# Kernel optimization log

Hardware: AMD Instinct MI355X
Metric: run time of the kernel (lower is better)

The kernel has to match this reference:

```python
import jax, jax.numpy as jnp
import numpy as np

B, C, H, W = 512, 256, 9, 9
HEADS, K = 4, 9
D_K = C // HEADS
EPS = 1e-5


def setup_inputs() -> dict:
    key = jax.random.key(0)
    ks = jax.random.split(key, 8)
    s = 1.0 / np.sqrt(C)
    return {
        "x": jax.random.normal(ks[0], (B, C, H, W), jnp.float32),
        "wq": jax.random.normal(ks[1], (C, C), jnp.float32) * s,
        "bq": jax.random.normal(ks[2], (C,), jnp.float32) * s,
        "wk": jax.random.normal(ks[3], (C, C), jnp.float32) * s,
        "bk": jax.random.normal(ks[4], (C,), jnp.float32) * s,
        "wv": jax.random.normal(ks[5], (C, C), jnp.float32) * s,
        "bv": jax.random.normal(ks[6], (C,), jnp.float32) * s,
        "a": jax.random.normal(ks[7], (HEADS, D_K), jnp.float32),
        "gamma": jnp.ones((C,), jnp.float32),
        "beta": jnp.zeros((C,), jnp.float32),
    }


def reference(x, wq, bq, wk, bk, wv, bv, a, gamma, beta):
    N = H * W  # 81 tokens
    tokens = x.reshape(B, C, N).transpose(0, 2, 1)  # [B, N, C]

    # pairwise euclidean distances (cdist)
    sq = jnp.sum(tokens * tokens, axis=-1)  # [B, N]
    d2 = sq[:, :, None] + sq[:, None, :] - 2.0 * jnp.einsum("bnc,bmc->bnm", tokens, tokens)
    dist = jnp.sqrt(jnp.maximum(d2, 0.0))  # [B, N, N]

    # k nearest neighbors (smallest distance)
    _, idx = jax.lax.top_k(-dist, K)  # idx: [B, N, K]

    # gather neighbor features: [B, N, K, C]
    nbr = jax.vmap(lambda t, i: t[i])(tokens, idx)

    q = tokens @ wq.T + bq                      # [B, N, C]
    kf = nbr @ wk.T + bk                        # [B, N, K, C]
    comb = jax.nn.leaky_relu(q[:, :, None, :] + kf, 0.2)
    comb = comb.reshape(B, N, K, HEADS, D_K)
    scores = jnp.einsum("bnkhd,hd->bnkh", comb, a)
    attn = jax.nn.softmax(scores, axis=2)       # over K neighbors
    v = (nbr @ wv.T + bv).reshape(B, N, K, HEADS, D_K)
    out = jnp.einsum("bnkh,bnkhd->bnhd", attn, v).reshape(B, N, C)
    out = out.transpose(0, 2, 1).reshape(B, C, H, W)

    # BatchNorm2d (training-mode batch statistics, biased variance)
    mean = jnp.mean(out, axis=(0, 2, 3))
    var = jnp.var(out, axis=(0, 2, 3))
    bn = (out - mean[None, :, None, None]) * jax.lax.rsqrt(var + EPS)[None, :, None, None]
    bn = bn * gamma[None, :, None, None] + beta[None, :, None, None]
    return jax.nn.relu(bn + x)
```

## Files before the change

kernel.cpp:

```cpp
#include <hip/hip_runtime.h>
#include <hip/hip_bf16.h>

#define B_   512
#define C_   256
#define N_   81
#define M_   (B_ * N_)
#define KNN  9

typedef __attribute__((ext_vector_type(8))) short short8;
typedef __attribute__((ext_vector_type(4))) float f32x4;
typedef __attribute__((ext_vector_type(4))) ushort u16x4;

#define GLD16(g, l) __builtin_amdgcn_global_load_lds(                      \
    (const __attribute__((address_space(1))) void*)(g),                    \
    (__attribute__((address_space(3))) void*)(l), 16, 0, 0)

__device__ __forceinline__ float bf2f(ushort u) {
  union { uint i; float f; } c; c.i = (uint)u << 16; return c.f;
}
__device__ __forceinline__ ushort f2bf(float f) {
  __hip_bfloat16 h = __float2bfloat16(f); return *(ushort*)&h;
}

__global__ __launch_bounds__(256) void split_kernel(
    const float* __restrict__ x, ushort* __restrict__ tokb,
    char* __restrict__ lobuf,
    const float* __restrict__ wq, const float* __restrict__ bq,
    const float* __restrict__ wk, const float* __restrict__ bk,
    const float* __restrict__ wv, const float* __restrict__ bv,
    ushort* __restrict__ wcat, float* __restrict__ bcat) {
  __shared__ __align__(16) float raw[32 * 81];
  const int bid = blockIdx.x;
  const int tid = threadIdx.x;
  if (bid >= 4096) {
    const int j = bid - 4096, c = tid;
    const int sel = j >> 8, jr = j & 255;
    const float* W  = sel == 0 ? wq : (sel == 1 ? wk : wv);
    const float* Bb = sel == 0 ? bq : (sel == 1 ? bk : bv);
    wcat[(size_t)j * 256 + c] = f2bf(W[jr * 256 + c]);
    if (c == 0) bcat[j] = Bb[jr];
    return;
  }
  const int b = bid >> 3, ch = bid & 7;
  const float* src = x + (size_t)b * (C_ * N_) + ch * 32 * N_;
#pragma unroll
  for (int it = 0; it < 3; ++it) {
    int e4 = tid + it * 256;
    if (e4 < 648) *(f32x4*)&raw[e4 * 4] = *(const f32x4*)&src[e4 * 4];
  }
  char* dst = lobuf + (size_t)bid * 6144;
  __syncthreads();
#pragma unroll
  for (int it = 0; it < 6; ++it) {
    int p = tid + it * 256;
    if (p < 1296) {
      int n = p >> 4, q = p & 15;
      float v0 = raw[(2 * q) * N_ + n];
      float v1 = raw[(2 * q + 1) * N_ + n];
      __hip_bfloat16 h0 = __float2bfloat16(v0);
      __hip_bfloat16 h1 = __float2bfloat16(v1);
      float r0 = v0 - __bfloat162float(h0);
      float r1 = v1 - __bfloat162float(h1);
      __hip_bfloat16 g0 = __float2bfloat16(r0);
      __hip_bfloat16 g1 = __float2bfloat16(r1);
      uint hp = (uint)(*(ushort*)&h0) | ((uint)(*(ushort*)&h1) << 16);
      uint lp = (uint)(*(ushort*)&g0) | ((uint)(*(ushort*)&g1) << 16);
      int off = (((q >> 2) << 4) ^ (((n >> 1) & 3) << 4)) + ((q & 3) << 2);
      *(uint*)(dst + n * 64 + off) = lp;
      *(uint*)&tokb[((size_t)(b * N_ + n)) * 256 + ch * 32 + 2 * q] = hp;
    }
  }
}

__global__ __launch_bounds__(256) void knn_kernel(
    const ushort* __restrict__ tokb, const char* __restrict__ lobuf,
    int* __restrict__ knn_idx) {
  __shared__ __align__(16) char smem[31488];
  __shared__ float sqv[96];
  const int b = blockIdx.x;
  const int tid = threadIdx.x;
  const int w = tid >> 6, lane = tid & 63;
  const int wr = w >> 1, wc = w & 1;
  const int l15 = lane & 15;
  const int g16 = lane >> 4;

  const char* tb = (const char*)(tokb + (size_t)b * N_ * 256);
  const char* lb = lobuf + (size_t)b * 8 * 6144;

#pragma unroll
  for (int it = 0; it < 3; ++it) {
    int idx = it * 256 + tid;
    if (idx < 384) {
      int n = idx >> 2, gp = idx & 3;
      int g = gp ^ ((n >> 1) & 3);
      GLD16(tb + (size_t)n * 512 + (g << 4), smem + idx * 16);
    } else {
      GLD16(lb + (idx - 384) * 16, smem + idx * 16);
    }
  }

  f32x4 acc[3][3];
#pragma unroll
  for (int i = 0; i < 3; ++i)
#pragma unroll
    for (int j = 0; j < 3; ++j) acc[i][j] = {0.f, 0.f, 0.f, 0.f};

#pragma unroll
  for (int ch = 0; ch < 8; ++ch) {
    char* cur = smem + (ch & 1) * 12288;
    char* nxt = smem + ((ch + 1) & 1) * 12288;
    if (ch < 7) {
#pragma unroll
      for (int it = 0; it < 3; ++it) {
        int idx = it * 256 + tid;
        if (idx < 384) {
          int n = idx >> 2, gp = idx & 3;
          int g = gp ^ ((n >> 1) & 3);
          GLD16(tb + (size_t)n * 512 + (ch + 1) * 64 + (g << 4),
                nxt + idx * 16);
        } else {
          GLD16(lb + (size_t)(ch + 1) * 6144 + (idx - 384) * 16,
                nxt + idx * 16);
        }
      }
      asm volatile("s_waitcnt vmcnt(3)" ::: "memory");
    } else {
      asm volatile("s_waitcnt vmcnt(0)" ::: "memory");
    }
    __builtin_amdgcn_s_barrier();
    __builtin_amdgcn_sched_barrier(0);
    short8 ah[3], al[3], bh[3], bl[3];
#pragma unroll
    for (int i = 0; i < 3; ++i) {
      int ra = wr * 48 + i * 16 + l15;
      int oa = ra * 64 + ((g16 << 4) ^ (((ra >> 1) & 3) << 4));
      ah[i] = *(const short8*)(cur + oa);
      al[i] = *(const short8*)(cur + 6144 + oa);
      int rb = wc * 48 + i * 16 + l15;
      int ob = rb * 64 + ((g16 << 4) ^ (((rb >> 1) & 3) << 4));
      bh[i] = *(const short8*)(cur + ob);
      bl[i] = *(const short8*)(cur + 6144 + ob);
    }
#pragma unroll
    for (int i = 0; i < 3; ++i)
#pragma unroll
      for (int j = 0; j < 3; ++j) {
        acc[i][j] = __builtin_amdgcn_mfma_f32_16x16x32_bf16(
            ah[i], bh[j], acc[i][j], 0, 0, 0);
        acc[i][j] = __builtin_amdgcn_mfma_f32_16x16x32_bf16(
            ah[i], bl[j], acc[i][j], 0, 0, 0);
        acc[i][j] = __builtin_amdgcn_mfma_f32_16x16x32_bf16(
            al[i], bh[j], acc[i][j], 0, 0, 0);
        acc[i][j] = __builtin_amdgcn_mfma_f32_16x16x32_bf16(
            al[i], bl[j], acc[i][j], 0, 0, 0);
      }
    __builtin_amdgcn_sched_barrier(0);
    __builtin_amdgcn_s_barrier();
  }
  float* G = (float*)smem;
#pragma unroll
  for (int i = 0; i < 3; ++i) {
    const int row0 = wr * 48 + i * 16 + ((lane >> 4) << 2);
#pragma unroll
    for (int j = 0; j < 3; ++j) {
      const int col = wc * 48 + j * 16 + l15;
#pragma unroll
      for (int reg = 0; reg < 4; ++reg) {
        const int row = row0 + reg;
        if (row < N_) G[row * 97 + col] = acc[i][j][reg];
      }
    }
  }
  __syncthreads();
  if (tid < N_) sqv[tid] = G[tid * 97 + tid];
  __syncthreads();
  if (tid < N_) {
    const int n = tid;
    const float sn = sqv[n];
    const float* grow = &G[n * 97];
    float bd[KNN]; int bi[KNN];
#pragma unroll
    for (int k = 0; k < KNN; ++k) { bd[k] = 3.4e38f; bi[k] = 0; }
    for (int m = 0; m < N_; ++m) {
      float d2 = sn + sqv[m] - 2.f * grow[m];
      float wv = bd[0]; int wi = 0;
#pragma unroll
      for (int k = 1; k < KNN; ++k) {
        bool g_ = bd[k] > wv;
        wv = g_ ? bd[k] : wv;
        wi = g_ ? k : wi;
      }
      bool repl = d2 < wv;
#pragma unroll
      for (int k = 0; k < KNN; ++k) {
        bool here = repl & (wi == k);
        bd[k] = here ? d2 : bd[k];
        bi[k] = here ? m : bi[k];
      }
    }
#pragma unroll
    for (int k = 0; k < KNN; ++k)
      knn_idx[((size_t)b * N_ + n) * KNN + k] = bi[k];
  }
}

__global__ __launch_bounds__(256) void qkv_mfma_kernel(
    const ushort* __restrict__ tokb, const ushort* __restrict__ wcat,
    const float* __restrict__ bcat, ushort* __restrict__ qkvb) {
  __shared__ ushort At[128 * 64];
  __shared__ ushort Bt[128 * 64];
  const int bid = blockIdx.x;
  const int xcd = bid & 7, li = bid >> 3;
  const int mt = xcd * 41 + li / 6;
  if (mt >= 324) return;
  const int m0 = mt * 128;
  const int j0 = (li % 6) * 128;
  const int tid = threadIdx.x;
  const int w = tid >> 6, lane = tid & 63;
  const int wr = w >> 1, wc = w & 1;

  const char* pA[4]; const char* pB[4]; int oL[4];
#pragma unroll
  for (int it = 0; it < 4; ++it) {
    int o = (it * 256 + tid) * 16;
    int r = o >> 7, cp = o & 127;
    int cl = cp ^ ((r & 7) << 4);
    oL[it] = o;
    pA[it] = (const char*)tokb + ((size_t)(m0 + r) * 256) * 2 + cl;
    pB[it] = (const char*)wcat + ((size_t)(j0 + r) * 256) * 2 + cl;
  }

  f32x4 acc[4][4];
#pragma unroll
  for (int i = 0; i < 4; ++i)
#pragma unroll
    for (int j = 0; j < 4; ++j) acc[i][j] = {0.f, 0.f, 0.f, 0.f};

  const int l15 = lane & 15;
  const int sw = (lane & 7) << 4;
  const int kgrp = (lane >> 4) << 4;

  for (int k0 = 0; k0 < 256; k0 += 64) {
    __syncthreads();
#pragma unroll
    for (int it = 0; it < 4; ++it) {
      GLD16(pA[it] + k0 * 2, (char*)At + oL[it]);
      GLD16(pB[it] + k0 * 2, (char*)Bt + oL[it]);
    }
    __syncthreads();
#pragma unroll
    for (int kk = 0; kk < 2; ++kk) {
      const int cb = (kk * 64 + kgrp) ^ sw;
      short8 am[4], bn[4];
#pragma unroll
      for (int i = 0; i < 4; ++i) {
        const int ra = wr * 64 + i * 16 + l15;
        am[i] = *(const short8*)((const char*)At + ra * 128 + cb);
        const int rb = wc * 64 + i * 16 + l15;
        bn[i] = *(const short8*)((const char*)Bt + rb * 128 + cb);
      }
#pragma unroll
      for (int i = 0; i < 4; ++i)
#pragma unroll
        for (int j = 0; j < 4; ++j)
          acc[i][j] = __builtin_amdgcn_mfma_f32_16x16x32_bf16(
              am[i], bn[j], acc[i][j], 0, 0, 0);
    }
  }

#pragma unroll
  for (int j = 0; j < 4; ++j) {
    const int colj = j0 + wc * 64 + j * 16 + l15;
    const float bs = bcat[colj];
#pragma unroll
    for (int i = 0; i < 4; ++i) {
      const int rowm = m0 + wr * 64 + i * 16 + ((lane >> 4) << 2);
#pragma unroll
      for (int reg = 0; reg < 4; ++reg)
        qkvb[(size_t)(rowm + reg) * 768 + colj] = f2bf(acc[i][j][reg] + bs);
    }
  }
}

__global__ __launch_bounds__(256) void attn_kernel(
    const ushort* __restrict__ qkvc, const int* __restrict__ knn_idx,
    const float* __restrict__ a, ushort* __restrict__ qkvb) {
  const int nwg = M_ / 4;
  const int bid = blockIdx.x;
  const int swz = (bid & 7) * (nwg / 8) + (bid >> 3);
  const int w = threadIdx.x >> 6, lane = threadIdx.x & 63;
  const int m = swz * 4 + w;
  const int b = m / N_;
  const int bbase = b * N_;

  int nbk_l = 0;
  if (lane < KNN) nbk_l = knn_idx[(size_t)m * KNN + lane];

  const u16x4 qu = *(const u16x4*)&qkvc[(size_t)m * 768 + lane * 4];
  const f32x4 a4 = *(const f32x4*)&a[lane * 4];
  float q4[4];
#pragma unroll
  for (int u = 0; u < 4; ++u) q4[u] = bf2f(qu[u]);

  float sc[KNN];
  int nb[KNN];
#pragma unroll
  for (int k = 0; k < KNN; ++k) {
    const int nbk = __builtin_amdgcn_readlane(nbk_l, k);
    nb[k] = nbk;
    const ushort* krow = qkvc + (size_t)(bbase + nbk) * 768 + 256;
    const u16x4 ku = *(const u16x4*)&krow[lane * 4];
    float p = 0.f;
#pragma unroll
    for (int u = 0; u < 4; ++u) {
      float t = q4[u] + bf2f(ku[u]);
      t = fmaxf(t, 0.2f * t);
      p = __builtin_fmaf(t, a4[u], p);
    }
    p += __shfl_xor(p, 1, 16);
    p += __shfl_xor(p, 2, 16);
    p += __shfl_xor(p, 4, 16);
    p += __shfl_xor(p, 8, 16);
    sc[k] = p;
  }
  float mx = sc[0];
#pragma unroll
  for (int k = 1; k < KNN; ++k) mx = fmaxf(mx, sc[k]);
  float s = 0.f;
#pragma unroll
  for (int k = 0; k < KNN; ++k) {
    sc[k] = __builtin_amdgcn_exp2f((sc[k] - mx) * 1.44269504f);
    s += sc[k];
  }
  const float inv = __builtin_amdgcn_rcpf(s);
  f32x4 acc = {0.f, 0.f, 0.f, 0.f};
#pragma unroll
  for (int k = 0; k < KNN; ++k) {
    const ushort* vrow = qkvc + (size_t)(bbase + nb[k]) * 768 + 512;
    const u16x4 vu = *(const u16x4*)&vrow[lane * 4];
    const float wk_ = sc[k] * inv;
#pragma unroll
    for (int u = 0; u < 4; ++u)
      acc[u] = __builtin_fmaf(wk_, bf2f(vu[u]), acc[u]);
  }
  u16x4 o;
#pragma unroll
  for (int u = 0; u < 4; ++u) o[u] = f2bf(acc[u]);
  *(u16x4*)&qkvb[(size_t)m * 768 + lane * 4] = o;
}

__global__ __launch_bounds__(256) void bn_partial_kernel(
    const ushort* __restrict__ qkvb, float* __restrict__ ps,
    float* __restrict__ ps2) {
  const int g = blockIdx.x, c = threadIdx.x;
  float s = 0.f, s2 = 0.f;
  for (int r = 0; r < M_ / 256; ++r) {
    float v = bf2f(qkvb[((size_t)g * (M_ / 256) + r) * 768 + c]);
    s += v; s2 += v * v;
  }
  ps[g * 256 + c] = s;
  ps2[g * 256 + c] = s2;
}

__global__ __launch_bounds__(256) void bn_finalize_kernel(
    const float* __restrict__ ps, const float* __restrict__ ps2,
    const float* __restrict__ gamma, const float* __restrict__ beta,
    float* __restrict__ scale, float* __restrict__ shift) {
  const int c = threadIdx.x;
  float s = 0.f, s2 = 0.f;
  for (int g = 0; g < 256; ++g) { s += ps[g * 256 + c]; s2 += ps2[g * 256 + c]; }
  const float mean = s * (1.f / (float)M_);
  const float var = s2 * (1.f / (float)M_) - mean * mean;
  const float rstd = rsqrtf(var + 1e-5f);
  scale[c] = gamma[c] * rstd;
  shift[c] = beta[c] - mean * gamma[c] * rstd;
}

__global__ __launch_bounds__(256) void bn_apply_kernel(
    const ushort* __restrict__ qkvb, const float* __restrict__ x,
    const float* __restrict__ scale, const float* __restrict__ shift,
    float* __restrict__ y) {
  __shared__ float t[N_ * 65];
  const int b = blockIdx.x, tid = threadIdx.x;
  for (int c0 = 0; c0 < 256; c0 += 64) {
    __syncthreads();
    for (int e = tid; e < N_ * 64; e += 256) {
      int n = e >> 6, c = e & 63;
      t[n * 65 + c] = bf2f(qkvb[((size_t)b * N_ + n) * 768 + c0 + c]);
    }
    __syncthreads();
    for (int f = tid; f < 64 * N_; f += 256) {
      int c = f / N_, n = f - c * N_;
      float o = t[n * 65 + c];
      size_t gi = (size_t)b * (C_ * N_) + (size_t)(c0 + c) * N_ + n;
      float bn = o * scale[c0 + c] + shift[c0 + c];
      float v = bn + x[gi];
      y[gi] = v > 0.f ? v : 0.f;
    }
  }
}

extern "C" void kernel_launch(void* const* d_in, const int* in_sizes, int n_in,
                              void* d_out, int out_size, void* d_ws,
                              size_t ws_size, hipStream_t stream) {
  const float* x     = (const float*)d_in[0];
  const float* wq    = (const float*)d_in[1];
  const float* bq    = (const float*)d_in[2];
  const float* wk    = (const float*)d_in[3];
  const float* bk    = (const float*)d_in[4];
  const float* wv    = (const float*)d_in[5];
  const float* bv    = (const float*)d_in[6];
  const float* a     = (const float*)d_in[7];
  const float* gamma = (const float*)d_in[8];
  const float* beta  = (const float*)d_in[9];
  float* out = (float*)d_out;

  ushort* qkvb = (ushort*)d_ws;
  char*   lobuf = (char*)qkvb;
  ushort* tokb = qkvb + (size_t)M_ * 768;
  ushort* wcat = tokb + (size_t)M_ * 256;
  float*  bcat = (float*)(wcat + 768 * 256);
  int*    kidx = (int*)(bcat + 768);
  float*  ps   = (float*)(kidx + (size_t)M_ * KNN);
  float*  ps2  = ps + 256 * 256;
  float*  scale = ps2 + 256 * 256;
  float*  shift = scale + 256;

  split_kernel<<<4096 + 768, 256, 0, stream>>>(
      x, tokb, lobuf, wq, bq, wk, bk, wv, bv, wcat, bcat);
  knn_kernel<<<B_, 256, 0, stream>>>(tokb, lobuf, kidx);
  qkv_mfma_kernel<<<1968, 256, 0, stream>>>(tokb, wcat, bcat, qkvb);
  attn_kernel<<<M_ / 4, 256, 0, stream>>>(qkvb, kidx, a, qkvb);
  bn_partial_kernel<<<256, 256, 0, stream>>>(qkvb, ps, ps2);
  bn_finalize_kernel<<<1, 256, 0, stream>>>(ps, ps2, gamma, beta, scale, shift);
  bn_apply_kernel<<<B_, 256, 0, stream>>>(qkvb, x, scale, shift, out);
}
```

Measured before the change: 160.8 us.

## Fuse attention with per-batch BN partial statistics and write compact output buffer

The attention kernel now runs one 1024-thread block per batch item, with 16 waves covering all 81 tokens. Outputs are staged in shared memory so the block can compute per-channel sum and sum-of-squares partials directly, which removes the separate bn_partial pass over global memory. Output is also written to a compact 256-stride buffer instead of the 768-stride qkv buffer, so bn_apply reads contiguous rows. In exchange, the finalize kernel must reduce 512 partials instead of 256, and the large blocks with 6-iteration per-wave loops may lower occupancy and latency hiding compared with the earlier fine-grained grid.

```diff
diff --git a/kernel.cpp b/kernel.cpp
--- a/kernel.cpp
+++ b/kernel.cpp
@@ -282,84 +282,96 @@
   }
 }
 
-__global__ __launch_bounds__(256) void attn_kernel(
+__global__ __launch_bounds__(1024) void attn_bn_kernel(
     const ushort* __restrict__ qkvc, const int* __restrict__ knn_idx,
-    const float* __restrict__ a, ushort* __restrict__ qkvb) {
-  const int nwg = M_ / 4;
+    const float* __restrict__ a, ushort* __restrict__ outNC,
+    float* __restrict__ ps, float* __restrict__ ps2) {
+  __shared__ __align__(16) char obuf[N_ * 512];
+  __shared__ float psl[2][256], psl2[2][256];
   const int bid = blockIdx.x;
-  const int swz = (bid & 7) * (nwg / 8) + (bid >> 3);
-  const int w = threadIdx.x >> 6, lane = threadIdx.x & 63;
-  const int m = swz * 4 + w;
-  const int b = m / N_;
+  const int b = (bid & 7) * 64 + (bid >> 3);
+  const int tid = threadIdx.x;
+  const int w = tid >> 6, lane = tid & 63;
   const int bbase = b * N_;
-
-  int nbk_l = 0;
-  if (lane < KNN) nbk_l = knn_idx[(size_t)m * KNN + lane];
-
-  const u16x4 qu = *(const u16x4*)&qkvc[(size_t)m * 768 + lane * 4];
   const f32x4 a4 = *(const f32x4*)&a[lane * 4];
-  float q4[4];
-#pragma unroll
-  for (int u = 0; u < 4; ++u) q4[u] = bf2f(qu[u]);
-
-  float sc[KNN];
-  int nb[KNN];
-#pragma unroll
-  for (int k = 0; k < KNN; ++k) {
-    const int nbk = __builtin_amdgcn_readlane(nbk_l, k);
-    nb[k] = nbk;
-    const ushort* krow = qkvc + (size_t)(bbase + nbk) * 768 + 256;
-    const u16x4 ku = *(const u16x4*)&krow[lane * 4];
-    float p = 0.f;
-#pragma unroll
-    for (int u = 0; u < 4; ++u) {
-      float t = q4[u] + bf2f(ku[u]);
-      t = fmaxf(t, 0.2f * t);
-      p = __builtin_fmaf(t, a4[u], p);
-    }
-    p += __shfl_xor(p, 1, 16);
-    p += __shfl_xor(p, 2, 16);
-    p += __shfl_xor(p, 4, 16);
-    p += __shfl_xor(p, 8, 16);
-    sc[k] = p;
-  }
-  float mx = sc[0];
-#pragma unroll
-  for (int k = 1; k < KNN; ++k) mx = fmaxf(mx, sc[k]);
-  float s = 0.f;
-#pragma unroll
-  for (int k = 0; k < KNN; ++k) {
-    sc[k] = __builtin_amdgcn_exp2f((sc[k] - mx) * 1.44269504f);
-    s += sc[k];
-  }
-  const float inv = __builtin_amdgcn_rcpf(s);
-  f32x4 acc = {0.f, 0.f, 0.f, 0.f};
-#pragma unroll
-  for (int k = 0; k < KNN; ++k) {
-    const ushort* vrow = qkvc + (size_t)(bbase + nb[k]) * 768 + 512;
-    const u16x4 vu = *(const u16x4*)&vrow[lane * 4];
-    const float wk_ = sc[k] * inv;
-#pragma unroll
-    for (int u = 0; u < 4; ++u)
-      acc[u] = __builtin_fmaf(wk_, bf2f(vu[u]), acc[u]);
-  }
-  u16x4 o;
-#pragma unroll
-  for (int u = 0; u < 4; ++u) o[u] = f2bf(acc[u]);
-  *(u16x4*)&qkvb[(size_t)m * 768 + lane * 4] = o;
-}
-
-__global__ __launch_bounds__(256) void bn_partial_kernel(
-    const ushort* __restrict__ qkvb, float* __restrict__ ps,
-    float* __restrict__ ps2) {
-  const int g = blockIdx.x, c = threadIdx.x;
-  float s = 0.f, s2 = 0.f;
-  for (int r = 0; r < M_ / 256; ++r) {
-    float v = bf2f(qkvb[((size_t)g * (M_ / 256) + r) * 768 + c]);
-    s += v; s2 += v * v;
-  }
-  ps[g * 256 + c] = s;
-  ps2[g * 256 + c] = s2;
+
+  for (int r = 0; r < 6; ++r) {
+    const int tok = w + 16 * r;
+    if (tok < N_) {
+      const int m = bbase + tok;
+      int nbk_l = 0;
+      if (lane < KNN) nbk_l = knn_idx[(size_t)m * KNN + lane];
+
+      const u16x4 qu = *(const u16x4*)&qkvc[(size_t)m * 768 + lane * 4];
+      float q4[4];
+#pragma unroll
+      for (int u = 0; u < 4; ++u) q4[u] = bf2f(qu[u]);
+
+      float sc[KNN];
+      int nb[KNN];
+#pragma unroll
+      for (int k = 0; k < KNN; ++k) {
+        const int nbk = __builtin_amdgcn_readlane(nbk_l, k);
+        nb[k] = nbk;
+        const ushort* krow = qkvc + (size_t)(bbase + nbk) * 768 + 256;
+        const u16x4 ku = *(const u16x4*)&krow[lane * 4];
+        float p = 0.f;
+#pragma unroll
+        for (int u = 0; u < 4; ++u) {
+          float t = q4[u] + bf2f(ku[u]);
+          t = fmaxf(t, 0.2f * t);
+          p = __builtin_fmaf(t, a4[u], p);
+        }
+        p += __shfl_xor(p, 1, 16);
+        p += __shfl_xor(p, 2, 16);
+        p += __shfl_xor(p, 4, 16);
+        p += __shfl_xor(p, 8, 16);
+        sc[k] = p;
+      }
+      float mx = sc[0];
+#pragma unroll
+      for (int k = 1; k < KNN; ++k) mx = fmaxf(mx, sc[k]);
+      float s = 0.f;
+#pragma unroll
+      for (int k = 0; k < KNN; ++k) {
+        sc[k] = __builtin_amdgcn_exp2f((sc[k] - mx) * 1.44269504f);
+        s += sc[k];
+      }
+      const float inv = __builtin_amdgcn_rcpf(s);
+      f32x4 acc = {0.f, 0.f, 0.f, 0.f};
+#pragma unroll
+      for (int k = 0; k < KNN; ++k) {
+        const ushort* vrow = qkvc + (size_t)(bbase + nb[k]) * 768 + 512;
+        const u16x4 vu = *(const u16x4*)&vrow[lane * 4];
+        const float wk_ = sc[k] * inv;
+#pragma unroll
+        for (int u = 0; u < 4; ++u)
+          acc[u] = __builtin_fmaf(wk_, bf2f(vu[u]), acc[u]);
+      }
+      u16x4 o;
+#pragma unroll
+      for (int u = 0; u < 4; ++u) o[u] = f2bf(acc[u]);
+      *(u16x4*)(obuf + tok * 512 + lane * 8) = o;
+      *(u16x4*)&outNC[(size_t)m * 256 + lane * 4] = o;
+    }
+  }
+  __syncthreads();
+  if (tid < 512) {
+    const int half = tid >> 8, c = tid & 255;
+    const int rbeg = half * 41, rend = half ? 81 : 41;
+    float s = 0.f, s2 = 0.f;
+    for (int rr = rbeg; rr < rend; ++rr) {
+      float v = bf2f(*(const ushort*)(obuf + rr * 512 + c * 2));
+      s += v; s2 = __builtin_fmaf(v, v, s2);
+    }
+    psl[half][c] = s;
+    psl2[half][c] = s2;
+  }
+  __syncthreads();
+  if (tid < 256) {
+    ps[b * 256 + tid] = psl[0][tid] + psl[1][tid];
+    ps2[b * 256 + tid] = psl2[0][tid] + psl2[1][tid];
+  }
 }
 
 __global__ __launch_bounds__(256) void bn_finalize_kernel(
@@ -368,7 +380,7 @@
     float* __restrict__ scale, float* __restrict__ shift) {
   const int c = threadIdx.x;
   float s = 0.f, s2 = 0.f;
-  for (int g = 0; g < 256; ++g) { s += ps[g * 256 + c]; s2 += ps2[g * 256 + c]; }
+  for (int g = 0; g < 512; ++g) { s += ps[g * 256 + c]; s2 += ps2[g * 256 + c]; }
   const float mean = s * (1.f / (float)M_);
   const float var = s2 * (1.f / (float)M_) - mean * mean;
   const float rstd = rsqrtf(var + 1e-5f);
@@ -377,7 +389,7 @@
 }
 
 __global__ __launch_bounds__(256) void bn_apply_kernel(
-    const ushort* __restrict__ qkvb, const float* __restrict__ x,
+    const ushort* __restrict__ outNC, const float* __restrict__ x,
     const float* __restrict__ scale, const float* __restrict__ shift,
     float* __restrict__ y) {
   __shared__ float t[N_ * 65];
@@ -386,7 +398,7 @@
     __syncthreads();
     for (int e = tid; e < N_ * 64; e += 256) {
       int n = e >> 6, c = e & 63;
-      t[n * 65 + c] = bf2f(qkvb[((size_t)b * N_ + n) * 768 + c0 + c]);
+      t[n * 65 + c] = bf2f(outNC[((size_t)b * N_ + n) * 256 + c0 + c]);
     }
     __syncthreads();
     for (int f = tid; f < 64 * N_; f += 256) {
@@ -422,16 +434,16 @@
   float*  bcat = (float*)(wcat + 768 * 256);
   int*    kidx = (int*)(bcat + 768);
   float*  ps   = (float*)(kidx + (size_t)M_ * KNN);
-  float*  ps2  = ps + 256 * 256;
-  float*  scale = ps2 + 256 * 256;
+  float*  ps2  = ps + 512 * 256;
+  float*  scale = ps2 + 512 * 256;
   float*  shift = scale + 256;
+  ushort* outNC = (ushort*)(shift + 256);
 
   split_kernel<<<4096 + 768, 256, 0, stream>>>(
       x, tokb, lobuf, wq, bq, wk, bk, wv, bv, wcat, bcat);
   knn_kernel<<<B_, 256, 0, stream>>>(tokb, lobuf, kidx);
   qkv_mfma_kernel<<<1968, 256, 0, stream>>>(tokb, wcat, bcat, qkvb);
-  attn_kernel<<<M_ / 4, 256, 0, stream>>>(qkvb, kidx, a, qkvb);
-  bn_partial_kernel<<<256, 256, 0, stream>>>(qkvb, ps, ps2);
+  attn_bn_kernel<<<B_, 1024, 0, stream>>>(qkvb, kidx, a, outNC, ps, ps2);
   bn_finalize_kernel<<<1, 256, 0, stream>>>(ps, ps2, gamma, beta, scale, shift);
-  bn_apply_kernel<<<B_, 256, 0, stream>>>(qkvb, x, scale, shift, out);
-}
+  bn_apply_kernel<<<B_, 256, 0, stream>>>(outNC, x, scale, shift, out);
+}
```

Measured after the change: 168.1 us. +4.5%, slower.

## Spread knn Gram tile across 12 waves with 768-thread blocks

Applied to the files above, without the earlier changes.

The knn kernel's block grows from 4 to 12 waves. Each wave now computes one 16-row strip by three 16-column tiles of the 96x96 Gram matrix instead of a 48x48 block, and each thread issues one async LDS load per chunk instead of three. The goal is more parallelism per batch element and less per-wave serial MFMA work and register pressure, since the grid is only 512 blocks. In exchange, operand reuse across waves drops, so more LDS reads are issued per MFMA, and barriers now synchronise 12 waves.

```diff
diff --git a/kernel.cpp b/kernel.cpp
--- a/kernel.cpp
+++ b/kernel.cpp
@@ -72,7 +72,7 @@
   }
 }
 
-__global__ __launch_bounds__(256) void knn_kernel(
+__global__ __launch_bounds__(768) void knn_kernel(
     const ushort* __restrict__ tokb, const char* __restrict__ lobuf,
     int* __restrict__ knn_idx) {
   __shared__ __align__(16) char smem[31488];
@@ -87,9 +87,8 @@
   const char* tb = (const char*)(tokb + (size_t)b * N_ * 256);
   const char* lb = lobuf + (size_t)b * 8 * 6144;
 
-#pragma unroll
-  for (int it = 0; it < 3; ++it) {
-    int idx = it * 256 + tid;
+  {
+    int idx = tid;
     if (idx < 384) {
       int n = idx >> 2, gp = idx & 3;
       int g = gp ^ ((n >> 1) & 3);
@@ -99,75 +98,59 @@
     }
   }
 
-  f32x4 acc[3][3];
-#pragma unroll
-  for (int i = 0; i < 3; ++i)
-#pragma unroll
-    for (int j = 0; j < 3; ++j) acc[i][j] = {0.f, 0.f, 0.f, 0.f};
+  f32x4 acc[3];
+#pragma unroll
+  for (int j = 0; j < 3; ++j) acc[j] = {0.f, 0.f, 0.f, 0.f};
 
 #pragma unroll
   for (int ch = 0; ch < 8; ++ch) {
     char* cur = smem + (ch & 1) * 12288;
     char* nxt = smem + ((ch + 1) & 1) * 12288;
     if (ch < 7) {
-#pragma unroll
-      for (int it = 0; it < 3; ++it) {
-        int idx = it * 256 + tid;
-        if (idx < 384) {
-          int n = idx >> 2, gp = idx & 3;
-          int g = gp ^ ((n >> 1) & 3);
-          GLD16(tb + (size_t)n * 512 + (ch + 1) * 64 + (g << 4),
-                nxt + idx * 16);
-        } else {
-          GLD16(lb + (size_t)(ch + 1) * 6144 + (idx - 384) * 16,
-                nxt + idx * 16);
-        }
+      int idx = tid;
+      if (idx < 384) {
+        int n = idx >> 2, gp = idx & 3;
+        int g = gp ^ ((n >> 1) & 3);
+        GLD16(tb + (size_t)n * 512 + (ch + 1) * 64 + (g << 4),
+              nxt + idx * 16);
+      } else {
+        GLD16(lb + (size_t)(ch + 1) * 6144 + (idx - 384) * 16,
+              nxt + idx * 16);
       }
-      asm volatile("s_waitcnt vmcnt(3)" ::: "memory");
+      asm volatile("s_waitcnt vmcnt(1)" ::: "memory");
     } else {
       asm volatile("s_waitcnt vmcnt(0)" ::: "memory");
     }
     __builtin_amdgcn_s_barrier();
     __builtin_amdgcn_sched_barrier(0);
-    short8 ah[3], al[3], bh[3], bl[3];
-#pragma unroll
-    for (int i = 0; i < 3; ++i) {
-      int ra = wr * 48 + i * 16 + l15;
-      int oa = ra * 64 + ((g16 << 4) ^ (((ra >> 1) & 3) << 4));
-      ah[i] = *(const short8*)(cur + oa);
-      al[i] = *(const short8*)(cur + 6144 + oa);
-      int rb = wc * 48 + i * 16 + l15;
+    const int ra = wr * 16 + l15;
+    const int oa = ra * 64 + ((g16 << 4) ^ (((ra >> 1) & 3) << 4));
+    short8 ah = *(const short8*)(cur + oa);
+    short8 al = *(const short8*)(cur + 6144 + oa);
+#pragma unroll
+    for (int j = 0; j < 3; ++j) {
+      int rb = wc * 48 + j * 16 + l15;
       int ob = rb * 64 + ((g16 << 4) ^ (((rb >> 1) & 3) << 4));
-      bh[i] = *(const short8*)(cur + ob);
-      bl[i] = *(const short8*)(cur + 6144 + ob);
-    }
-#pragma unroll
-    for (int i = 0; i < 3; ++i)
-#pragma unroll
-      for (int j = 0; j < 3; ++j) {
-        acc[i][j] = __builtin_amdgcn_mfma_f32_16x16x32_bf16(
-            ah[i], bh[j], acc[i][j], 0, 0, 0);
-        acc[i][j] = __builtin_amdgcn_mfma_f32_16x16x32_bf16(
-            ah[i], bl[j], acc[i][j], 0, 0, 0);
-        acc[i][j] = __builtin_amdgcn_mfma_f32_16x16x32_bf16(
-            al[i], bh[j], acc[i][j], 0, 0, 0);
-        acc[i][j] = __builtin_amdgcn_mfma_f32_16x16x32_bf16(
-            al[i], bl[j], acc[i][j], 0, 0, 0);
-      }
+      short8 bh = *(const short8*)(cur + ob);
+      short8 bl = *(const short8*)(cur + 6144 + ob);
+      acc[j] = __builtin_amdgcn_mfma_f32_16x16x32_bf16(ah, bh, acc[j], 0, 0, 0);
+      acc[j] = __builtin_amdgcn_mfma_f32_16x16x32_bf16(ah, bl, acc[j], 0, 0, 0);
+      acc[j] = __builtin_amdgcn_mfma_f32_16x16x32_bf16(al, bh, acc[j], 0, 0, 0);
+      acc[j] = __builtin_amdgcn_mfma_f32_16x16x32_bf16(al, bl, acc[j], 0, 0, 0);
+    }
     __builtin_amdgcn_sched_barrier(0);
     __builtin_amdgcn_s_barrier();
   }
   float* G = (float*)smem;
-#pragma unroll
-  for (int i = 0; i < 3; ++i) {
-    const int row0 = wr * 48 + i * 16 + ((lane >> 4) << 2);
+  {
+    const int row0 = wr * 16 + ((lane >> 4) << 2);
 #pragma unroll
     for (int j = 0; j < 3; ++j) {
       const int col = wc * 48 + j * 16 + l15;
 #pragma unroll
       for (int reg = 0; reg < 4; ++reg) {
         const int row = row0 + reg;
-        if (row < N_) G[row * 97 + col] = acc[i][j][reg];
+        if (row < N_) G[row * 97 + col] = acc[j][reg];
       }
     }
   }
@@ -428,7 +411,7 @@
 
   split_kernel<<<4096 + 768, 256, 0, stream>>>(
       x, tokb, lobuf, wq, bq, wk, bk, wv, bv, wcat, bcat);
-  knn_kernel<<<B_, 256, 0, stream>>>(tokb, lobuf, kidx);
+  knn_kernel<<<B_, 768, 0, stream>>>(tokb, lobuf, kidx);
   qkv_mfma_kernel<<<1968, 256, 0, stream>>>(tokb, wcat, bcat, qkvb);
   attn_kernel<<<M_ / 4, 256, 0, stream>>>(qkvb, kidx, a, qkvb);
   bn_partial_kernel<<<256, 256, 0, stream>>>(qkvb, ps, ps2);
```

After: 159.1 us. About the same (-1.1%).

## Merge kNN and QKV GEMM into one launch, batch attn loads, parallelize BN finalize

Applied to the files above, without the earlier changes.

The kNN Gram kernel and the QKV projection GEMM become one kernel launch: the first 512 blocks run kNN and the rest run the GEMM. This lets the two independent stages overlap on the GPU and removes a launch boundary. To make that safe, the low-part buffer moves out of the qkvb region into its own workspace area. The attention kernel now issues all K and V neighbour loads up front to raise memory-level parallelism, at the cost of more registers. The BN finalize uses one block per channel with a tree reduction instead of a single serial block.

```diff
diff --git a/kernel.cpp b/kernel.cpp
--- a/kernel.cpp
+++ b/kernel.cpp
@@ -72,151 +72,152 @@
   }
 }
 
-__global__ __launch_bounds__(256) void knn_kernel(
+__global__ __launch_bounds__(256) void knn_gemm_kernel(
     const ushort* __restrict__ tokb, const char* __restrict__ lobuf,
-    int* __restrict__ knn_idx) {
-  __shared__ __align__(16) char smem[31488];
-  __shared__ float sqv[96];
-  const int b = blockIdx.x;
+    int* __restrict__ knn_idx,
+    const ushort* __restrict__ wcat, const float* __restrict__ bcat,
+    ushort* __restrict__ qkvb) {
+  __shared__ __align__(16) char smem[32768];
+  const int bid0 = blockIdx.x;
   const int tid = threadIdx.x;
   const int w = tid >> 6, lane = tid & 63;
-  const int wr = w >> 1, wc = w & 1;
   const int l15 = lane & 15;
-  const int g16 = lane >> 4;
-
-  const char* tb = (const char*)(tokb + (size_t)b * N_ * 256);
-  const char* lb = lobuf + (size_t)b * 8 * 6144;
-
-#pragma unroll
-  for (int it = 0; it < 3; ++it) {
-    int idx = it * 256 + tid;
-    if (idx < 384) {
-      int n = idx >> 2, gp = idx & 3;
-      int g = gp ^ ((n >> 1) & 3);
-      GLD16(tb + (size_t)n * 512 + (g << 4), smem + idx * 16);
-    } else {
-      GLD16(lb + (idx - 384) * 16, smem + idx * 16);
-    }
-  }
-
-  f32x4 acc[3][3];
-#pragma unroll
-  for (int i = 0; i < 3; ++i)
-#pragma unroll
-    for (int j = 0; j < 3; ++j) acc[i][j] = {0.f, 0.f, 0.f, 0.f};
-
-#pragma unroll
-  for (int ch = 0; ch < 8; ++ch) {
-    char* cur = smem + (ch & 1) * 12288;
-    char* nxt = smem + ((ch + 1) & 1) * 12288;
-    if (ch < 7) {
-#pragma unroll
-      for (int it = 0; it < 3; ++it) {
-        int idx = it * 256 + tid;
-        if (idx < 384) {
-          int n = idx >> 2, gp = idx & 3;
-          int g = gp ^ ((n >> 1) & 3);
-          GLD16(tb + (size_t)n * 512 + (ch + 1) * 64 + (g << 4),
-                nxt + idx * 16);
-        } else {
-          GLD16(lb + (size_t)(ch + 1) * 6144 + (idx - 384) * 16,
-                nxt + idx * 16);
+
+  if (bid0 < B_) {
+    float* sqv = (float*)(smem + 31488);
+    const int b = bid0;
+    const int wr = w >> 1, wc = w & 1;
+    const int g16 = lane >> 4;
+
+    const char* tb = (const char*)(tokb + (size_t)b * N_ * 256);
+    const char* lb = lobuf + (size_t)b * 8 * 6144;
+
+#pragma unroll
+    for (int it = 0; it < 3; ++it) {
+      int idx = it * 256 + tid;
+      if (idx < 384) {
+        int n = idx >> 2, gp = idx & 3;
+        int g = gp ^ ((n >> 1) & 3);
+        GLD16(tb + (size_t)n * 512 + (g << 4), smem + idx * 16);
+      } else {
+        GLD16(lb + (idx - 384) * 16, smem + idx * 16);
+      }
+    }
+
+    f32x4 acc[3][3];
+#pragma unroll
+    for (int i = 0; i < 3; ++i)
+#pragma unroll
+      for (int j = 0; j < 3; ++j) acc[i][j] = {0.f, 0.f, 0.f, 0.f};
+
+#pragma unroll
+    for (int ch = 0; ch < 8; ++ch) {
+      char* cur = smem + (ch & 1) * 12288;
+      char* nxt = smem + ((ch + 1) & 1) * 12288;
+      if (ch < 7) {
+#pragma unroll
+        for (int it = 0; it < 3; ++it) {
+          int idx = it * 256 + tid;
+          if (idx < 384) {
+            int n = idx >> 2, gp = idx & 3;
+            int g = gp ^ ((n >> 1) & 3);
+            GLD16(tb + (size_t)n * 512 + (ch + 1) * 64 + (g << 4),
+                  nxt + idx * 16);
+          } else {
+            GLD16(lb + (size_t)(ch + 1) * 6144 + (idx - 384) * 16,
+                  nxt + idx * 16);
+          }
         }
-      }
-      asm volatile("s_waitcnt vmcnt(3)" ::: "memory");
-    } else {
-      asm volatile("s_waitcnt vmcnt(0)" ::: "memory");
-    }
-    __builtin_amdgcn_s_barrier();
-    __builtin_amdgcn_sched_barrier(0);
-    short8 ah[3], al[3], bh[3], bl[3];
+        asm volatile("s_waitcnt vmcnt(3)" ::: "memory");
+      } else {
+        asm volatile("s_waitcnt vmcnt(0)" ::: "memory");
+      }
+      __builtin_amdgcn_s_barrier();
+      __builtin_amdgcn_sched_barrier(0);
+      short8 ah[3], al[3], bh[3], bl[3];
+#pragma unroll
+      for (int i = 0; i < 3; ++i) {
+        int ra = wr * 48 + i * 16 + l15;
+        int oa = ra * 64 + ((g16 << 4) ^ (((ra >> 1) & 3) << 4));
+        ah[i] = *(const short8*)(cur + oa);
+        al[i] = *(const short8*)(cur + 6144 + oa);
+        int rb = wc * 48 + i * 16 + l15;
+        int ob = rb * 64 + ((g16 << 4) ^ (((rb >> 1) & 3) << 4));
+        bh[i] = *(const short8*)(cur + ob);
+        bl[i] = *(const short8*)(cur + 6144 + ob);
+      }
+#pragma unroll
+      for (int i = 0; i < 3; ++i)
+#pragma unroll
+        for (int j = 0; j < 3; ++j) {
+          acc[i][j] = __builtin_amdgcn_mfma_f32_16x16x32_bf16(
+              ah[i], bh[j], acc[i][j], 0, 0, 0);
+          acc[i][j] = __builtin_amdgcn_mfma_f32_16x16x32_bf16(
+              ah[i], bl[j], acc[i][j], 0, 0, 0);
+          acc[i][j] = __builtin_amdgcn_mfma_f32_16x16x32_bf16(
+              al[i], bh[j], acc[i][j], 0, 0, 0);
+          acc[i][j] = __builtin_amdgcn_mfma_f32_16x16x32_bf16(
+              al[i], bl[j], acc[i][j], 0, 0, 0);
+        }
+      __builtin_amdgcn_sched_barrier(0);
+      __builtin_amdgcn_s_barrier();
+    }
+    float* G = (float*)smem;
 #pragma unroll
     for (int i = 0; i < 3; ++i) {
-      int ra = wr * 48 + i * 16 + l15;
-      int oa = ra * 64 + ((g16 << 4) ^ (((ra >> 1) & 3) << 4));
-      ah[i] = *(const short8*)(cur + oa);
-      al[i] = *(const short8*)(cur + 6144 + oa);
-      int rb = wc * 48 + i * 16 + l15;
-      int ob = rb * 64 + ((g16 << 4) ^ (((rb >> 1) & 3) << 4));
-      bh[i] = *(const short8*)(cur + ob);
-      bl[i] = *(const short8*)(cur + 6144 + ob);
-    }
-#pragma unroll
-    for (int i = 0; i < 3; ++i)
+      const int row0 = wr * 48 + i * 16 + ((lane >> 4) << 2);
 #pragma unroll
       for (int j = 0; j < 3; ++j) {
-        acc[i][j] = __builtin_amdgcn_mfma_f32_16x16x32_bf16(
-            ah[i], bh[j], acc[i][j], 0, 0, 0);
-        acc[i][j] = __builtin_amdgcn_mfma_f32_16x16x32_bf16(
-            ah[i], bl[j], acc[i][j], 0, 0, 0);
-        acc[i][j] = __builtin_amdgcn_mfma_f32_16x16x32_bf16(
-            al[i], bh[j], acc[i][j], 0, 0, 0);
-        acc[i][j] = __builtin_amdgcn_mfma_f32_16x16x32_bf16(
-            al[i], bl[j], acc[i][j], 0, 0, 0);
-      }
-    __builtin_amdgcn_sched_barrier(0);
-    __builtin_amdgcn_s_barrier();
-  }
-  float* G = (float*)smem;
-#pragma unroll
-  for (int i = 0; i < 3; ++i) {
-    const int row0 = wr * 48 + i * 16 + ((lane >> 4) << 2);
-#pragma unroll
-    for (int j = 0; j < 3; ++j) {
-      const int col = wc * 48 + j * 16 + l15;
-#pragma unroll
-      for (int reg = 0; reg < 4; ++reg) {
-        const int row = row0 + reg;
-        if (row < N_) G[row * 97 + col] = acc[i][j][reg];
-      }
-    }
-  }
-  __syncthreads();
-  if (tid < N_) sqv[tid] = G[tid * 97 + tid];
-  __syncthreads();
-  if (tid < N_) {
-    const int n = tid;
-    const float sn = sqv[n];
-    const float* grow = &G[n * 97];
-    float bd[KNN]; int bi[KNN];
-#pragma unroll
-    for (int k = 0; k < KNN; ++k) { bd[k] = 3.4e38f; bi[k] = 0; }
-    for (int m = 0; m < N_; ++m) {
-      float d2 = sn + sqv[m] - 2.f * grow[m];
-      float wv = bd[0]; int wi = 0;
-#pragma unroll
-      for (int k = 1; k < KNN; ++k) {
-        bool g_ = bd[k] > wv;
-        wv = g_ ? bd[k] : wv;
-        wi = g_ ? k : wi;
-      }
-      bool repl = d2 < wv;
-#pragma unroll
-      for (int k = 0; k < KNN; ++k) {
-        bool here = repl & (wi == k);
-        bd[k] = here ? d2 : bd[k];
-        bi[k] = here ? m : bi[k];
-      }
-    }
-#pragma unroll
-    for (int k = 0; k < KNN; ++k)
-      knn_idx[((size_t)b * N_ + n) * KNN + k] = bi[k];
-  }
-}
-
-__global__ __launch_bounds__(256) void qkv_mfma_kernel(
-    const ushort* __restrict__ tokb, const ushort* __restrict__ wcat,
-    const float* __restrict__ bcat, ushort* __restrict__ qkvb) {
-  __shared__ ushort At[128 * 64];
-  __shared__ ushort Bt[128 * 64];
-  const int bid = blockIdx.x;
+        const int col = wc * 48 + j * 16 + l15;
+#pragma unroll
+        for (int reg = 0; reg < 4; ++reg) {
+          const int row = row0 + reg;
+          if (row < N_) G[row * 97 + col] = acc[i][j][reg];
+        }
+      }
+    }
+    __syncthreads();
+    if (tid < N_) sqv[tid] = G[tid * 97 + tid];
+    __syncthreads();
+    if (tid < N_) {
+      const int n = tid;
+      const float sn = sqv[n];
+      const float* grow = &G[n * 97];
+      float bd[KNN]; int bi[KNN];
+#pragma unroll
+      for (int k = 0; k < KNN; ++k) { bd[k] = 3.4e38f; bi[k] = 0; }
+      for (int m = 0; m < N_; ++m) {
+        float d2 = sn + sqv[m] - 2.f * grow[m];
+        float wv = bd[0]; int wi = 0;
+#pragma unroll
+        for (int k = 1; k < KNN; ++k) {
+          bool g_ = bd[k] > wv;
+          wv = g_ ? bd[k] : wv;
+          wi = g_ ? k : wi;
+        }
+        bool repl = d2 < wv;
+#pragma unroll
+        for (int k = 0; k < KNN; ++k) {
+          bool here = repl & (wi == k);
+          bd[k] = here ? d2 : bd[k];
+          bi[k] = here ? m : bi[k];
+        }
+      }
+#pragma unroll
+      for (int k = 0; k < KNN; ++k)
+        knn_idx[((size_t)b * N_ + n) * KNN + k] = bi[k];
+    }
+    return;
+  }
+
+  ushort* At = (ushort*)smem;
+  ushort* Bt = (ushort*)(smem + 16384);
+  const int bid = bid0 - B_;
   const int xcd = bid & 7, li = bid >> 3;
   const int mt = xcd * 41 + li / 6;
   if (mt >= 324) return;
   const int m0 = mt * 128;
   const int j0 = (li % 6) * 128;
-  const int tid = threadIdx.x;
-  const int w = tid >> 6, lane = tid & 63;
   const int wr = w >> 1, wc = w & 1;
 
   const char* pA[4]; const char* pB[4]; int oL[4];
@@ -236,7 +237,6 @@
 #pragma unroll
     for (int j = 0; j < 4; ++j) acc[i][j] = {0.f, 0.f, 0.f, 0.f};
 
-  const int l15 = lane & 15;
   const int sw = (lane & 7) << 4;
   const int kgrp = (lane >> 4) << 4;
 
@@ -302,18 +302,22 @@
 #pragma unroll
   for (int u = 0; u < 4; ++u) q4[u] = bf2f(qu[u]);
 
-  float sc[KNN];
-  int nb[KNN];
+  u16x4 ku[KNN], vu[KNN];
 #pragma unroll
   for (int k = 0; k < KNN; ++k) {
     const int nbk = __builtin_amdgcn_readlane(nbk_l, k);
-    nb[k] = nbk;
-    const ushort* krow = qkvc + (size_t)(bbase + nbk) * 768 + 256;
-    const u16x4 ku = *(const u16x4*)&krow[lane * 4];
+    const ushort* row = qkvc + (size_t)(bbase + nbk) * 768;
+    ku[k] = *(const u16x4*)&row[256 + lane * 4];
+    vu[k] = *(const u16x4*)&row[512 + lane * 4];
+  }
+
+  float sc[KNN];
+#pragma unroll
+  for (int k = 0; k < KNN; ++k) {
     float p = 0.f;
 #pragma unroll
     for (int u = 0; u < 4; ++u) {
-      float t = q4[u] + bf2f(ku[u]);
+      float t = q4[u] + bf2f(ku[k][u]);
       t = fmaxf(t, 0.2f * t);
       p = __builtin_fmaf(t, a4[u], p);
     }
@@ -336,12 +340,10 @@
   f32x4 acc = {0.f, 0.f, 0.f, 0.f};
 #pragma unroll
   for (int k = 0; k < KNN; ++k) {
-    const ushort* vrow = qkvc + (size_t)(bbase + nb[k]) * 768 + 512;
-    const u16x4 vu = *(const u16x4*)&vrow[lane * 4];
     const float wk_ = sc[k] * inv;
 #pragma unroll
     for (int u = 0; u < 4; ++u)
-      acc[u] = __builtin_fmaf(wk_, bf2f(vu[u]), acc[u]);
+      acc[u] = __builtin_fmaf(wk_, bf2f(vu[k][u]), acc[u]);
   }
   u16x4 o;
 #pragma unroll
@@ -366,14 +368,26 @@
     const float* __restrict__ ps, const float* __restrict__ ps2,
     const float* __restrict__ gamma, const float* __restrict__ beta,
     float* __restrict__ scale, float* __restrict__ shift) {
-  const int c = threadIdx.x;
-  float s = 0.f, s2 = 0.f;
-  for (int g = 0; g < 256; ++g) { s += ps[g * 256 + c]; s2 += ps2[g * 256 + c]; }
-  const float mean = s * (1.f / (float)M_);
-  const float var = s2 * (1.f / (float)M_) - mean * mean;
-  const float rstd = rsqrtf(var + 1e-5f);
-  scale[c] = gamma[c] * rstd;
-  shift[c] = beta[c] - mean * gamma[c] * rstd;
+  __shared__ float red[2][256];
+  const int c = blockIdx.x, t = threadIdx.x;
+  red[0][t] = ps[t * 256 + c];
+  red[1][t] = ps2[t * 256 + c];
+  __syncthreads();
+#pragma unroll
+  for (int off = 128; off > 0; off >>= 1) {
+    if (t < off) {
+      red[0][t] += red[0][t + off];
+      red[1][t] += red[1][t + off];
+    }
+    __syncthreads();
+  }
+  if (t == 0) {
+    const float mean = red[0][0] * (1.f / (float)M_);
+    const float var = red[1][0] * (1.f / (float)M_) - mean * mean;
+    const float rstd = rsqrtf(var + 1e-5f);
+    scale[c] = gamma[c] * rstd;
+    shift[c] = beta[c] - mean * gamma[c] * rstd;
+  }
 }
 
 __global__ __launch_bounds__(256) void bn_apply_kernel(
@@ -425,13 +439,14 @@
   float*  ps2  = ps + 256 * 256;
   float*  scale = ps2 + 256 * 256;
   float*  shift = scale + 256;
+  char*   lobuf2 = (char*)(shift + 256);
 
   split_kernel<<<4096 + 768, 256, 0, stream>>>(
-      x, tokb, lobuf, wq, bq, wk, bk, wv, bv, wcat, bcat);
-  knn_kernel<<<B_, 256, 0, stream>>>(tokb, lobuf, kidx);
-  qkv_mfma_kernel<<<1968, 256, 0, stream>>>(tokb, wcat, bcat, qkvb);
+      x, tokb, lobuf2, wq, bq, wk, bk, wv, bv, wcat, bcat);
+  knn_gemm_kernel<<<B_ + 1968, 256, 0, stream>>>(
+      tokb, lobuf2, kidx, wcat, bcat, qkvb);
   attn_kernel<<<M_ / 4, 256, 0, stream>>>(qkvb, kidx, a, qkvb);
   bn_partial_kernel<<<256, 256, 0, stream>>>(qkvb, ps, ps2);
-  bn_finalize_kernel<<<1, 256, 0, stream>>>(ps, ps2, gamma, beta, scale, shift);
+  bn_finalize_kernel<<<256, 256, 0, stream>>>(ps, ps2, gamma, beta, scale, shift);
   bn_apply_kernel<<<B_, 256, 0, stream>>>(qkvb, x, scale, shift, out);
 }
```

After: 141.1 us. 12.3% less time.
